# Optimization experiments

Measured on AMD Instinct MI355X. Metric: run time of the kernel, lower is better.

Reference implementation:

```python
import jax, jax.numpy as jnp
import numpy as np

NUM_HEADS = 4
WORD_DIM = 100
LEAKY_ALPHA = 0.3  # keras LeakyReLU default negative_slope


def setup_inputs() -> dict:
    key = jax.random.key(0)
    k1, k2, k3 = jax.random.split(key, 3)
    x = jax.random.normal(k1, (8, 30, 20, 40, WORD_DIM), dtype=jnp.float32)
    # keras 'random_normal' initializer: stddev 0.05
    w_att = jax.random.normal(k2, (NUM_HEADS, WORD_DIM), dtype=jnp.float32) * 0.05
    b_att = jax.random.normal(k3, (NUM_HEADS, WORD_DIM), dtype=jnp.float32) * 0.05
    return {"x": x, "w_att": w_att, "b_att": b_att}


def reference(x, w_att, b_att):
    # x: [B, T, E, W, D]; w_att, b_att: [H, D]
    B, T, E, W, D = x.shape
    H = w_att.shape[0]
    type_emb = x[..., 0, :]        # [B,T,E,D]
    words = x[..., 1:, :]          # [B,T,E,N,D], N = W-1
    # per-head hidden representation: leaky_relu(w*words + b)
    pre = words[..., None, :, :] * w_att[:, None, :] + b_att[:, None, :]  # [B,T,E,H,N,D]
    hidden = jnp.where(pre >= 0, pre, LEAKY_ALPHA * pre)
    # attention scores: dot(type_emb, hidden) over D
    scores = jnp.einsum('bted,btehnd->btehn', type_emb, hidden)  # [B,T,E,H,N]
    # original uses raw exp / sum (no max-subtraction) -- keep faithful
    att = jnp.exp(scores)
    att = att / jnp.sum(att, axis=-1, keepdims=True)
    out = jnp.einsum('btehn,btend->bthed'.replace('bthed', 'btehd'), att, words)  # [B,T,E,H,D]
    out = out.reshape(B, T, E, H * D)
    # all-zero events map to zero embeddings
    nonzero = jnp.any(x != 0, axis=(-1, -2), keepdims=False)  # [B,T,E]
    out = jnp.where(nonzero[..., None], out, 0.0)
    return out
```

## Files before the change

kernel.cpp:

```cpp
#include <hip/hip_runtime.h>
#include <math.h>
#include <stdint.h>

#define NHEAD 4
#define DD 100
#define NW 39
#define BLOCK 256
#define ALPHA 0.3f

typedef __attribute__((address_space(3))) uint32_t lds_t;
typedef const __attribute__((address_space(1))) uint32_t glb_t;

__global__ __launch_bounds__(BLOCK, 6) void ts_enc(
    const float* __restrict__ x,
    const float* __restrict__ w_att,
    const float* __restrict__ b_att,
    float* __restrict__ out)
{
    __shared__ float tile[40 * DD];
    __shared__ float sc_part[4][40][4];
    __shared__ float att_T[40][4];
    __shared__ float pcs[NHEAD][4][25][4];

    const int tid  = threadIdx.x;
    const int wv   = __builtin_amdgcn_readfirstlane(tid >> 6);
    const int lane = tid & 63;
    const float* xsite = x + (size_t)blockIdx.x * (40 * DD);

    #pragma unroll
    for (int i = 0; i < 4; ++i) {
        const int cf = i * BLOCK + tid;
        if (cf < 1000) {
            glb_t* g = (glb_t*)(xsite + cf * 4);
            lds_t* l = (lds_t*)(tile + (i * BLOCK + wv * 64) * 4);
            __builtin_amdgcn_global_load_lds(g, l, 16, 0, 0);
        }
    }
    __syncthreads();

    const bool act = (lane < NW);
    const float* wrow = tile + (1 + lane) * DD;
    float acc[NHEAD] = {0.f, 0.f, 0.f, 0.f};

    for (int c = wv; c < 25; c += 4) {
        const float4 te4 = *(const float4*)(xsite + c * 4);
        float4 v4 = make_float4(0.f, 0.f, 0.f, 0.f);
        if (act) v4 = *(const float4*)(wrow + c * 4);

        #pragma unroll
        for (int h = 0; h < NHEAD; ++h) {
            const float4 w4 = *(const float4*)(w_att + h * DD + c * 4);
            const float4 b4 = *(const float4*)(b_att + h * DD + c * 4);
            float p0 = fmaf(v4.x, w4.x, b4.x);
            float p1 = fmaf(v4.y, w4.y, b4.y);
            float p2 = fmaf(v4.z, w4.z, b4.z);
            float p3 = fmaf(v4.w, w4.w, b4.w);
            p0 = fmaxf(p0, 0.f) + ALPHA * fminf(p0, 0.f);
            p1 = fmaxf(p1, 0.f) + ALPHA * fminf(p1, 0.f);
            p2 = fmaxf(p2, 0.f) + ALPHA * fminf(p2, 0.f);
            p3 = fmaxf(p3, 0.f) + ALPHA * fminf(p3, 0.f);
            float d = fmaf(te4.x, p0, fmaf(te4.y, p1, fmaf(te4.z, p2, te4.w * p3)));
            acc[h] += d;
        }
    }
    if (act)
        *(float4*)&sc_part[wv][lane][0] = make_float4(acc[0], acc[1], acc[2], acc[3]);
    __syncthreads();

    float sc = -INFINITY;
    if (act)
        sc = sc_part[0][lane][wv] + sc_part[1][lane][wv]
           + sc_part[2][lane][wv] + sc_part[3][lane][wv];
    float mx = sc;
    #pragma unroll
    for (int off = 32; off; off >>= 1) mx = fmaxf(mx, __shfl_xor(mx, off));
    float p = act ? __expf(sc - mx) : 0.f;
    float sm = p;
    #pragma unroll
    for (int off = 32; off; off >>= 1) sm += __shfl_xor(sm, off);
    if (act) att_T[lane][wv] = p / sm;
    __syncthreads();

    if (tid < 100) {
        const int ng = tid / 25;
        const int dc = tid - ng * 25;
        const int n0 = ng * 10;
        const int n1 = (ng == 3) ? NW : n0 + 10;
        float4 ac0 = {0,0,0,0}, ac1 = {0,0,0,0}, ac2 = {0,0,0,0}, ac3 = {0,0,0,0};
        const float* cb = tile + DD + dc * 4;
        for (int n = n0; n < n1; ++n) {
            const float4 wd = *(const float4*)(cb + n * DD);
            const float4 at = *(const float4*)&att_T[n][0];
            ac0.x = fmaf(at.x, wd.x, ac0.x); ac0.y = fmaf(at.x, wd.y, ac0.y);
            ac0.z = fmaf(at.x, wd.z, ac0.z); ac0.w = fmaf(at.x, wd.w, ac0.w);
            ac1.x = fmaf(at.y, wd.x, ac1.x); ac1.y = fmaf(at.y, wd.y, ac1.y);
            ac1.z = fmaf(at.y, wd.z, ac1.z); ac1.w = fmaf(at.y, wd.w, ac1.w);
            ac2.x = fmaf(at.z, wd.x, ac2.x); ac2.y = fmaf(at.z, wd.y, ac2.y);
            ac2.z = fmaf(at.z, wd.z, ac2.z); ac2.w = fmaf(at.z, wd.w, ac2.w);
            ac3.x = fmaf(at.w, wd.x, ac3.x); ac3.y = fmaf(at.w, wd.y, ac3.y);
            ac3.z = fmaf(at.w, wd.z, ac3.z); ac3.w = fmaf(at.w, wd.w, ac3.w);
        }
        *(float4*)&pcs[0][ng][dc][0] = ac0;
        *(float4*)&pcs[1][ng][dc][0] = ac1;
        *(float4*)&pcs[2][ng][dc][0] = ac2;
        *(float4*)&pcs[3][ng][dc][0] = ac3;
    }
    __syncthreads();

    if (tid < 100) {
        const int h  = tid / 25;
        const int dc = tid - h * 25;
        const float4 q0 = *(const float4*)&pcs[h][0][dc][0];
        const float4 q1 = *(const float4*)&pcs[h][1][dc][0];
        const float4 q2 = *(const float4*)&pcs[h][2][dc][0];
        const float4 q3 = *(const float4*)&pcs[h][3][dc][0];
        float4 r;
        r.x = (q0.x + q1.x) + (q2.x + q3.x);
        r.y = (q0.y + q1.y) + (q2.y + q3.y);
        r.z = (q0.z + q1.z) + (q2.z + q3.z);
        r.w = (q0.w + q1.w) + (q2.w + q3.w);
        *(float4*)(out + (size_t)blockIdx.x * (NHEAD * DD) + h * DD + dc * 4) = r;
    }
}

extern "C" void kernel_launch(void* const* d_in, const int* in_sizes, int n_in,
                              void* d_out, int out_size, void* d_ws, size_t ws_size,
                              hipStream_t stream) {
    const float* x     = (const float*)d_in[0];
    const float* w_att = (const float*)d_in[1];
    const float* b_att = (const float*)d_in[2];
    float* out = (float*)d_out;

    const int sites = 8 * 30 * 20;
    ts_enc<<<sites, BLOCK, 0, stream>>>(x, w_att, b_att, out);
}
```

Before: 32.02 us.

## Process four sites per block with double-buffered LDS prefetch and per-wave weighted sum

Each block now handles four consecutive sites, prefetching the next site's tile into a second LDS buffer via global_load_lds while computing the current one, using explicit vmcnt waits and raw barriers. The weighted-sum phase is restructured so each wave owns one head and uses lane shuffles for attention weights, replacing the cross-head partial buffers and extra barriers. The aim is to hide global load latency and remove synchronization steps. In exchange the grid shrinks to a quarter, occupancy bound drops, and correctness relies on hand-written waitcnt counts matching the async loads.

```diff
diff --git a/kernel.cpp b/kernel.cpp
--- a/kernel.cpp
+++ b/kernel.cpp
@@ -6,120 +6,120 @@
 #define DD 100
 #define NW 39
 #define BLOCK 256
+#define NS 4
 #define ALPHA 0.3f
 
 typedef __attribute__((address_space(3))) uint32_t lds_t;
 typedef const __attribute__((address_space(1))) uint32_t glb_t;
 
-__global__ __launch_bounds__(BLOCK, 6) void ts_enc(
+__device__ __forceinline__ void stage_tile(const float* xs, float* buf, int tid, int wv) {
+#pragma unroll
+    for (int i = 0; i < 4; ++i) {
+        const int cf = i * BLOCK + tid;
+        if (cf < 1000) {
+            glb_t* g = (glb_t*)(xs + cf * 4);
+            lds_t* l = (lds_t*)(buf + (i * BLOCK + wv * 64) * 4);
+            __builtin_amdgcn_global_load_lds(g, l, 16, 0, 0);
+        }
+    }
+}
+
+__global__ __launch_bounds__(BLOCK, 4) void ts_enc(
     const float* __restrict__ x,
     const float* __restrict__ w_att,
     const float* __restrict__ b_att,
     float* __restrict__ out)
 {
-    __shared__ float tile[40 * DD];
-    __shared__ float sc_part[4][40][4];
-    __shared__ float att_T[40][4];
-    __shared__ float pcs[NHEAD][4][25][4];
+    __shared__ float tile[2][40 * DD];
+    __shared__ float scp[NHEAD][4][40];
 
     const int tid  = threadIdx.x;
     const int wv   = __builtin_amdgcn_readfirstlane(tid >> 6);
     const int lane = tid & 63;
-    const float* xsite = x + (size_t)blockIdx.x * (40 * DD);
+    const int site0 = blockIdx.x * NS;
 
-    #pragma unroll
-    for (int i = 0; i < 4; ++i) {
-        const int cf = i * BLOCK + tid;
-        if (cf < 1000) {
-            glb_t* g = (glb_t*)(xsite + cf * 4);
-            lds_t* l = (lds_t*)(tile + (i * BLOCK + wv * 64) * 4);
-            __builtin_amdgcn_global_load_lds(g, l, 16, 0, 0);
+    stage_tile(x + (size_t)site0 * (40 * DD), tile[0], tid, wv);
+
+#pragma unroll
+    for (int s = 0; s < NS; ++s) {
+        const int site = site0 + s;
+        const float* tile_s = tile[s & 1];
+
+        if (s == 0) { asm volatile("s_waitcnt vmcnt(0)" ::: "memory"); }
+        else        { asm volatile("s_waitcnt vmcnt(1)" ::: "memory"); }
+        __builtin_amdgcn_s_barrier();
+        __builtin_amdgcn_sched_barrier(0);
+
+        if (s + 1 < NS)
+            stage_tile(x + (size_t)(site + 1) * (40 * DD), tile[(s + 1) & 1], tid, wv);
+        __builtin_amdgcn_sched_barrier(0);
+
+        const bool act = lane < NW;
+        const float* wrow = tile_s + (1 + lane) * DD;
+        float acc[NHEAD] = {0.f, 0.f, 0.f, 0.f};
+        for (int c = wv; c < 25; c += 4) {
+            const float4 te4 = *(const float4*)(tile_s + c * 4);
+            float4 v4 = make_float4(0.f, 0.f, 0.f, 0.f);
+            if (act) v4 = *(const float4*)(wrow + c * 4);
+            #pragma unroll
+            for (int h = 0; h < NHEAD; ++h) {
+                const float4 w4 = *(const float4*)(w_att + h * DD + c * 4);
+                const float4 b4 = *(const float4*)(b_att + h * DD + c * 4);
+                float p0 = fmaf(v4.x, w4.x, b4.x);
+                float p1 = fmaf(v4.y, w4.y, b4.y);
+                float p2 = fmaf(v4.z, w4.z, b4.z);
+                float p3 = fmaf(v4.w, w4.w, b4.w);
+                p0 = fmaxf(p0, 0.f) + ALPHA * fminf(p0, 0.f);
+                p1 = fmaxf(p1, 0.f) + ALPHA * fminf(p1, 0.f);
+                p2 = fmaxf(p2, 0.f) + ALPHA * fminf(p2, 0.f);
+                p3 = fmaxf(p3, 0.f) + ALPHA * fminf(p3, 0.f);
+                acc[h] += fmaf(te4.x, p0, fmaf(te4.y, p1, fmaf(te4.z, p2, te4.w * p3)));
+            }
         }
-    }
-    __syncthreads();
+        if (act) {
+            scp[0][wv][lane] = acc[0];
+            scp[1][wv][lane] = acc[1];
+            scp[2][wv][lane] = acc[2];
+            scp[3][wv][lane] = acc[3];
+        }
+        asm volatile("s_waitcnt lgkmcnt(0)" ::: "memory");
+        __builtin_amdgcn_s_barrier();
+        __builtin_amdgcn_sched_barrier(0);
 
-    const bool act = (lane < NW);
-    const float* wrow = tile + (1 + lane) * DD;
-    float acc[NHEAD] = {0.f, 0.f, 0.f, 0.f};
+        float sc = -INFINITY;
+        if (act) sc = (scp[wv][0][lane] + scp[wv][1][lane])
+                    + (scp[wv][2][lane] + scp[wv][3][lane]);
+        float mx = sc;
+        #pragma unroll
+        for (int off = 32; off; off >>= 1) mx = fmaxf(mx, __shfl_xor(mx, off));
+        float p = act ? __expf(sc - mx) : 0.f;
+        float sm = p;
+        #pragma unroll
+        for (int off = 32; off; off >>= 1) sm += __shfl_xor(sm, off);
+        const float a = p / sm;
 
-    for (int c = wv; c < 25; c += 4) {
-        const float4 te4 = *(const float4*)(xsite + c * 4);
-        float4 v4 = make_float4(0.f, 0.f, 0.f, 0.f);
-        if (act) v4 = *(const float4*)(wrow + c * 4);
-
+        const int half = lane >> 5;
+        const int dc   = lane & 31;
+        const int dcc  = dc < 25 ? dc : 24;
+        float4 ca = make_float4(0.f, 0.f, 0.f, 0.f);
+        const float* wb = tile_s + DD + dcc * 4;
         #pragma unroll
-        for (int h = 0; h < NHEAD; ++h) {
-            const float4 w4 = *(const float4*)(w_att + h * DD + c * 4);
-            const float4 b4 = *(const float4*)(b_att + h * DD + c * 4);
-            float p0 = fmaf(v4.x, w4.x, b4.x);
-            float p1 = fmaf(v4.y, w4.y, b4.y);
-            float p2 = fmaf(v4.z, w4.z, b4.z);
-            float p3 = fmaf(v4.w, w4.w, b4.w);
-            p0 = fmaxf(p0, 0.f) + ALPHA * fminf(p0, 0.f);
-            p1 = fmaxf(p1, 0.f) + ALPHA * fminf(p1, 0.f);
-            p2 = fmaxf(p2, 0.f) + ALPHA * fminf(p2, 0.f);
-            p3 = fmaxf(p3, 0.f) + ALPHA * fminf(p3, 0.f);
-            float d = fmaf(te4.x, p0, fmaf(te4.y, p1, fmaf(te4.z, p2, te4.w * p3)));
-            acc[h] += d;
+        for (int i = 0; i < 20; ++i) {
+            const int n  = half * 20 + i;
+            const int nn = n < NW ? n : NW - 1;
+            const float attn = __shfl(a, n);
+            const float4 wd = *(const float4*)(wb + nn * DD);
+            ca.x = fmaf(attn, wd.x, ca.x);
+            ca.y = fmaf(attn, wd.y, ca.y);
+            ca.z = fmaf(attn, wd.z, ca.z);
+            ca.w = fmaf(attn, wd.w, ca.w);
         }
-    }
-    if (act)
-        *(float4*)&sc_part[wv][lane][0] = make_float4(acc[0], acc[1], acc[2], acc[3]);
-    __syncthreads();
-
-    float sc = -INFINITY;
-    if (act)
-        sc = sc_part[0][lane][wv] + sc_part[1][lane][wv]
-           + sc_part[2][lane][wv] + sc_part[3][lane][wv];
-    float mx = sc;
-    #pragma unroll
-    for (int off = 32; off; off >>= 1) mx = fmaxf(mx, __shfl_xor(mx, off));
-    float p = act ? __expf(sc - mx) : 0.f;
-    float sm = p;
-    #pragma unroll
-    for (int off = 32; off; off >>= 1) sm += __shfl_xor(sm, off);
-    if (act) att_T[lane][wv] = p / sm;
-    __syncthreads();
-
-    if (tid < 100) {
-        const int ng = tid / 25;
-        const int dc = tid - ng * 25;
-        const int n0 = ng * 10;
-        const int n1 = (ng == 3) ? NW : n0 + 10;
-        float4 ac0 = {0,0,0,0}, ac1 = {0,0,0,0}, ac2 = {0,0,0,0}, ac3 = {0,0,0,0};
-        const float* cb = tile + DD + dc * 4;
-        for (int n = n0; n < n1; ++n) {
-            const float4 wd = *(const float4*)(cb + n * DD);
-            const float4 at = *(const float4*)&att_T[n][0];
-            ac0.x = fmaf(at.x, wd.x, ac0.x); ac0.y = fmaf(at.x, wd.y, ac0.y);
-            ac0.z = fmaf(at.x, wd.z, ac0.z); ac0.w = fmaf(at.x, wd.w, ac0.w);
-            ac1.x = fmaf(at.y, wd.x, ac1.x); ac1.y = fmaf(at.y, wd.y, ac1.y);
-            ac1.z = fmaf(at.y, wd.z, ac1.z); ac1.w = fmaf(at.y, wd.w, ac1.w);
-            ac2.x = fmaf(at.z, wd.x, ac2.x); ac2.y = fmaf(at.z, wd.y, ac2.y);
-            ac2.z = fmaf(at.z, wd.z, ac2.z); ac2.w = fmaf(at.z, wd.w, ac2.w);
-            ac3.x = fmaf(at.w, wd.x, ac3.x); ac3.y = fmaf(at.w, wd.y, ac3.y);
-            ac3.z = fmaf(at.w, wd.z, ac3.z); ac3.w = fmaf(at.w, wd.w, ac3.w);
-        }
-        *(float4*)&pcs[0][ng][dc][0] = ac0;
-        *(float4*)&pcs[1][ng][dc][0] = ac1;
-        *(float4*)&pcs[2][ng][dc][0] = ac2;
-        *(float4*)&pcs[3][ng][dc][0] = ac3;
-    }
-    __syncthreads();
-
-    if (tid < 100) {
-        const int h  = tid / 25;
-        const int dc = tid - h * 25;
-        const float4 q0 = *(const float4*)&pcs[h][0][dc][0];
-        const float4 q1 = *(const float4*)&pcs[h][1][dc][0];
-        const float4 q2 = *(const float4*)&pcs[h][2][dc][0];
-        const float4 q3 = *(const float4*)&pcs[h][3][dc][0];
-        float4 r;
-        r.x = (q0.x + q1.x) + (q2.x + q3.x);
-        r.y = (q0.y + q1.y) + (q2.y + q3.y);
-        r.z = (q0.z + q1.z) + (q2.z + q3.z);
-        r.w = (q0.w + q1.w) + (q2.w + q3.w);
-        *(float4*)(out + (size_t)blockIdx.x * (NHEAD * DD) + h * DD + dc * 4) = r;
+        ca.x += __shfl_xor(ca.x, 32);
+        ca.y += __shfl_xor(ca.y, 32);
+        ca.z += __shfl_xor(ca.z, 32);
+        ca.w += __shfl_xor(ca.w, 32);
+        if (half == 0 && dc < 25)
+            *(float4*)(out + (size_t)site * (NHEAD * DD) + wv * DD + dc * 4) = ca;
     }
 }
 
@@ -132,5 +132,5 @@
     float* out = (float*)d_out;
 
     const int sites = 8 * 30 * 20;
-    ts_enc<<<sites, BLOCK, 0, stream>>>(x, w_att, b_att, out);
+    ts_enc<<<sites / NS, BLOCK, 0, stream>>>(x, w_att, b_att, out);
 }
```

Result: slower. 43.90 us (+37.1%).
